# Optimization experiments

Hardware: AMD Instinct MI355X
Metric: run time of the kernel (lower is better)

The kernel has to match this reference:

```python
import jax, jax.numpy as jnp
import numpy as np

N_NODES = 100000
N_EDGES = 1200000
N_GRAPHS = 512
F_IN = 7
H = 64
N_CLASSES = 10


def _xavier(key, shape):
    fan_in, fan_out = shape[0], shape[1]
    limit = float(np.sqrt(6.0 / (fan_in + fan_out)))
    return jax.random.uniform(key, shape, jnp.float32, -limit, limit)


def setup_inputs() -> dict:
    key = jax.random.key(0)
    ks = jax.random.split(key, 16)
    x = jax.random.normal(ks[0], (N_NODES, F_IN), jnp.float32)
    edge_index = jax.random.randint(ks[1], (2, N_EDGES), 0, N_NODES, jnp.int64)
    batch = jnp.sort(jax.random.randint(ks[2], (N_NODES,), 0, N_GRAPHS, jnp.int64))
    d = {
        'x': x, 'edge_index': edge_index, 'batch': batch,
        'W_emb': _xavier(ks[3], (F_IN, H)), 'b_emb': jnp.zeros((H,), jnp.float32),
        'eps1': jnp.zeros((), jnp.float32),
        'W1a': _xavier(ks[4], (H, 2 * H)), 'b1a': jnp.zeros((2 * H,), jnp.float32),
        'W1b': _xavier(ks[5], (2 * H, H)), 'b1b': jnp.zeros((H,), jnp.float32),
        'eps2': jnp.zeros((), jnp.float32),
        'W2a': _xavier(ks[6], (H, 2 * H)), 'b2a': jnp.zeros((2 * H,), jnp.float32),
        'W2b': _xavier(ks[7], (2 * H, H)), 'b2b': jnp.zeros((H,), jnp.float32),
        'eps3': jnp.zeros((), jnp.float32),
        'W3a': _xavier(ks[8], (H, 2 * H)), 'b3a': jnp.zeros((2 * H,), jnp.float32),
        'W3b': _xavier(ks[9], (2 * H, H)), 'b3b': jnp.zeros((H,), jnp.float32),
        'Wc1': _xavier(ks[10], (2 * H, H)), 'bc1': jnp.zeros((H,), jnp.float32),
        'Wc2': _xavier(ks[11], (H, N_CLASSES)), 'bc2': jnp.zeros((N_CLASSES,), jnp.float32),
    }
    return d


def _gin_layer(x, eps, Wa, ba, Wb, bb, src, dst):
    # scatter-add aggregation of source features into destination nodes
    agg = jax.ops.segment_sum(x[src], dst, num_segments=N_NODES)
    h = (1.0 + eps) * x + agg
    h = jax.nn.relu(h @ Wa + ba) @ Wb + bb
    return jax.nn.elu(h)  # dropout is identity in eval mode


def reference(x, edge_index, batch,
              W_emb, b_emb,
              eps1, W1a, b1a, W1b, b1b,
              eps2, W2a, b2a, W2b, b2b,
              eps3, W3a, b3a, W3b, b3b,
              Wc1, bc1, Wc2, bc2):
    src, dst = edge_index[0], edge_index[1]
    h = x @ W_emb + b_emb                      # [N, H]
    h = _gin_layer(h, eps1, W1a, b1a, W1b, b1b, src, dst)
    h = _gin_layer(h, eps2, W2a, b2a, W2b, b2b, src, dst)
    h = _gin_layer(h, eps3, W3a, b3a, W3b, b3b, src, dst)
    # global mean + max pool per graph
    sums = jax.ops.segment_sum(h, batch, num_segments=N_GRAPHS)
    cnts = jax.ops.segment_sum(jnp.ones((h.shape[0], 1), h.dtype), batch, num_segments=N_GRAPHS)
    mean = sums / jnp.maximum(cnts, 1.0)
    mx = jax.ops.segment_max(h, batch, num_segments=N_GRAPHS)
    g = jnp.concatenate([mean, mx], axis=1)    # [G, 2H]
    out = jax.nn.relu(g @ Wc1 + bc1) @ Wc2 + bc2
    return out
```

## Files before the change

kernel.cpp:

```cpp
#include <hip/hip_runtime.h>
#include <hip/hip_bf16.h>
#include <math.h>

#define N_NODES 100000
#define N_EDGES 1200000
#define N_GRAPHS 512
#define NBUCKET 196
#define BSHIFT 9
#define TILE 2048
#define CSR_CAP 8192

typedef __bf16 bf16x8 __attribute__((ext_vector_type(8)));
typedef float f32x4 __attribute__((ext_vector_type(4)));

__device__ __forceinline__ unsigned f2ord(float f) {
  unsigned u = __float_as_uint(f);
  return (u & 0x80000000u) ? ~u : (u | 0x80000000u);
}
__device__ __forceinline__ float ord2f(unsigned u) {
  return (u & 0x80000000u) ? __uint_as_float(u & 0x7fffffffu) : __uint_as_float(~u);
}

__global__ void bucket_hist_kernel(const int* __restrict__ dst, int* __restrict__ bcnt) {
  __shared__ int c[256];
  int t = threadIdx.x;
  c[t] = 0;
  __syncthreads();
  for (int e = blockIdx.x * 256 + t; e < N_EDGES; e += gridDim.x * 256)
    atomicAdd(&c[dst[e] >> BSHIFT], 1);
  __syncthreads();
  if (t < NBUCKET && c[t] > 0) atomicAdd(&bcnt[t], c[t]);
}

__global__ void bucket_scan_kernel(const int* __restrict__ bcnt,
                                   int* __restrict__ bbase,
                                   int* __restrict__ bcursor,
                                   int* __restrict__ rowp) {
  __shared__ int s[256];
  int t = threadIdx.x;
  int own = (t < NBUCKET) ? bcnt[t] : 0;
  s[t] = own;
  __syncthreads();
  for (int o = 1; o < 256; o <<= 1) {
    int v = (t >= o) ? s[t - o] : 0;
    __syncthreads();
    s[t] += v;
    __syncthreads();
  }
  if (t < NBUCKET) {
    int excl = s[t] - own;
    bbase[t] = excl;
    bcursor[t] = excl;
  }
  if (t == 0) {
    bbase[NBUCKET] = N_EDGES;
    rowp[N_NODES] = N_EDGES;
  }
}

__global__ void partition_kernel(const int* __restrict__ src, const int* __restrict__ dst,
                                 int* __restrict__ bcursor, unsigned* __restrict__ ent) {
  __shared__ int cnt[256];
  __shared__ int cnt2[256];
  __shared__ int lstart[256];
  __shared__ int gbase[256];
  __shared__ int s[256];
  __shared__ unsigned sorted[TILE];
  __shared__ unsigned char bid[TILE];
  int t = threadIdx.x;
  int e0 = blockIdx.x * TILE;
  cnt[t] = 0; cnt2[t] = 0;
  __syncthreads();

  unsigned v[8];
  int b[8];
#pragma unroll
  for (int u = 0; u < 8; ++u) {
    int e = e0 + u * 256 + t;
    b[u] = -1;
    if (e < N_EDGES) {
      int d = dst[e];
      b[u] = d >> BSHIFT;
      v[u] = (unsigned)src[e] | ((unsigned)(d & 511) << 17);
      atomicAdd(&cnt[b[u]], 1);
    }
  }
  __syncthreads();
  s[t] = cnt[t];
  __syncthreads();
  for (int o = 1; o < 256; o <<= 1) {
    int x = (t >= o) ? s[t - o] : 0;
    __syncthreads();
    s[t] += x;
    __syncthreads();
  }
  lstart[t] = s[t] - cnt[t];
  __syncthreads();
  if (t < NBUCKET) gbase[t] = (cnt[t] > 0) ? atomicAdd(&bcursor[t], cnt[t]) : 0;
  __syncthreads();
#pragma unroll
  for (int u = 0; u < 8; ++u) {
    if (b[u] >= 0) {
      int p = lstart[b[u]] + atomicAdd(&cnt2[b[u]], 1);
      sorted[p] = v[u];
      bid[p] = (unsigned char)b[u];
    }
  }
  __syncthreads();
  int ntile = min(TILE, N_EDGES - e0);
  for (int i = t; i < ntile; i += 256) {
    int bb = bid[i];
    ent[gbase[bb] + (i - lstart[bb])] = sorted[i];
  }
}

__launch_bounds__(256)
__global__ void bucket_csr_kernel(const unsigned* __restrict__ ent,
                                  const int* __restrict__ bbase,
                                  int* __restrict__ rowp,
                                  int* __restrict__ ssrc) {
  __shared__ unsigned le[CSR_CAP];
  __shared__ int deg[512];
  __shared__ int excl[512];
  __shared__ int ws[256];
  int t = threadIdx.x;
  int b = blockIdx.x;
  int base = bbase[b];
  int cntb = bbase[b + 1] - base;
  deg[t] = 0; deg[t + 256] = 0;
  __syncthreads();
  for (int i = t; i < cntb; i += 256) {
    unsigned e = ent[base + i];
    if (i < CSR_CAP) le[i] = e;
    atomicAdd(&deg[e >> 17], 1);
  }
  __syncthreads();
  int d0 = deg[t * 2], d1 = deg[t * 2 + 1];
  int sum2 = d0 + d1;
  ws[t] = sum2;
  __syncthreads();
  for (int o = 1; o < 256; o <<= 1) {
    int x = (t >= o) ? ws[t - o] : 0;
    __syncthreads();
    ws[t] += x;
    __syncthreads();
  }
  int run = ws[t] - sum2;
  excl[t * 2] = run; run += d0;
  excl[t * 2 + 1] = run;
  __syncthreads();
  int node0 = b << BSHIFT;
#pragma unroll
  for (int k = 0; k < 2; ++k) {
    int i = t * 2 + k;
    int n = node0 + i;
    if (n < N_NODES) rowp[n] = base + excl[i];
    deg[i] = excl[i];
  }
  __syncthreads();
  for (int i = t; i < cntb; i += 256) {
    unsigned e = (i < CSR_CAP) ? le[i] : ent[base + i];
    int p = atomicAdd(&deg[e >> 17], 1);
    ssrc[base + p] = (int)(e & 0x1FFFFu);
  }
}

__global__ void convert_all_kernel(const float* __restrict__ W1a, const float* __restrict__ W1b,
                                   const float* __restrict__ W2a, const float* __restrict__ W2b,
                                   const float* __restrict__ W3a, const float* __restrict__ W3b,
                                   __bf16* __restrict__ wp,
                                   float* gsum, unsigned* gmax, int* gcnt) {
  int o = blockIdx.x * 256 + threadIdx.x;
  if (o < N_GRAPHS * 64) {
    gsum[o] = 0.0f;
    gmax[o] = 0x407FFFFFu;
  }
  if (o < N_GRAPHS) gcnt[o] = 0;
  int L = o >> 14, q = o & 16383;
  const float* Wa = (L == 0) ? W1a : (L == 1) ? W2a : W3a;
  const float* Wb = (L == 0) ? W1b : (L == 1) ? W2b : W3b;
  if (q < 8192) {
    int j = q & 7, c = (q >> 3) & 15, kc = (q >> 7) & 3, kt = (q >> 9) & 1, nt = q >> 10;
    wp[o] = (__bf16)Wa[(kt * 32 + kc * 8 + j) * 128 + nt * 16 + c];
  } else {
    int p = q - 8192;
    int j = p & 7, c = (p >> 3) & 15, kc = (p >> 7) & 3, kt = (p >> 9) & 3, nt2 = p >> 11;
    wp[o] = (__bf16)Wb[(kt * 32 + kc * 8 + j) * 64 + nt2 * 16 + c];
  }
}

__device__ __forceinline__ void mlp_tail(const __bf16* AsW, __bf16* HsW,
                                         const __bf16* __restrict__ W1p,
                                         const float* __restrict__ b1,
                                         const __bf16* __restrict__ W2p,
                                         const float* __restrict__ b2,
                                         __bf16* __restrict__ hout,
                                         int n0b, int wv, int c, int kc, int m0) {
  bf16x8 a1_0 = *(const bf16x8*)&AsW[(m0 + c) * 72 + 0 * 32 + kc * 8];
  bf16x8 a1_1 = *(const bf16x8*)&AsW[(m0 + c) * 72 + 1 * 32 + kc * 8];
  f32x4 acc1[8];
#pragma unroll
  for (int nt = 0; nt < 8; ++nt) {
    float bv = b1[nt * 16 + c];
    f32x4 acc = {bv, bv, bv, bv};
    bf16x8 bf0 = *(const bf16x8*)&W1p[(nt * 2 + 0) * 512 + kc * 128 + c * 8];
    bf16x8 bf1 = *(const bf16x8*)&W1p[(nt * 2 + 1) * 512 + kc * 128 + c * 8];
    acc = __builtin_amdgcn_mfma_f32_16x16x32_bf16(a1_0, bf0, acc, 0, 0, 0);
    acc = __builtin_amdgcn_mfma_f32_16x16x32_bf16(a1_1, bf1, acc, 0, 0, 0);
    acc1[nt] = acc;
  }
#pragma unroll
  for (int nt = 0; nt < 8; ++nt) {
#pragma unroll
    for (int r = 0; r < 4; ++r) {
      HsW[(m0 + kc * 4 + r) * 136 + nt * 16 + c] = (__bf16)fmaxf(acc1[nt][r], 0.0f);
    }
  }
  bf16x8 a2[4];
#pragma unroll
  for (int kt = 0; kt < 4; ++kt)
    a2[kt] = *(const bf16x8*)&HsW[(m0 + c) * 136 + kt * 32 + kc * 8];
#pragma unroll
  for (int nt2 = 0; nt2 < 4; ++nt2) {
    float bv = b2[nt2 * 16 + c];
    f32x4 acc = {bv, bv, bv, bv};
#pragma unroll
    for (int kt = 0; kt < 4; ++kt) {
      bf16x8 bf = *(const bf16x8*)&W2p[(nt2 * 4 + kt) * 512 + kc * 128 + c * 8];
      acc = __builtin_amdgcn_mfma_f32_16x16x32_bf16(a2[kt], bf, acc, 0, 0, 0);
    }
#pragma unroll
    for (int r = 0; r < 4; ++r) {
      int g = n0b + m0 + kc * 4 + r;
      if (g < N_NODES) {
        float o = acc[r];
        hout[(size_t)g * 64 + nt2 * 16 + c] = (__bf16)((o > 0.0f) ? o : expm1f(o));
      }
    }
  }
}

__launch_bounds__(256)
__global__ void gin_fused_l1_kernel(const float* __restrict__ x,
                                    __bf16* __restrict__ hout,
                                    const int* __restrict__ row_ptr,
                                    const int* __restrict__ ssrc,
                                    const float* __restrict__ eps_p,
                                    const float* __restrict__ W_emb,
                                    const float* __restrict__ b_emb,
                                    const __bf16* __restrict__ W1p,
                                    const float* __restrict__ b1,
                                    const __bf16* __restrict__ W2p,
                                    const float* __restrict__ b2) {
  __shared__ __bf16 As[64 * 72];
  __shared__ __bf16 Hs[64 * 136];
  int t = threadIdx.x, lane = t & 63, wv = t >> 6;
  int c = lane & 15, kc = lane >> 4;
  int m0 = wv * 16;
  float epsv = 1.0f + eps_p[0];
  int n0b = blockIdx.x * 64;
  int n0w = n0b + m0;

  float w0 = W_emb[0 * 64 + lane], w1 = W_emb[1 * 64 + lane], w2 = W_emb[2 * 64 + lane];
  float w3 = W_emb[3 * 64 + lane], w4 = W_emb[4 * 64 + lane], w5 = W_emb[5 * 64 + lane];
  float w6 = W_emb[6 * 64 + lane];
  float bl = b_emb[lane];

  int rp = row_ptr[min(n0w + min(lane, 16), N_NODES)];

#define EDGE7(sv, acc) { \
    const float* xr = &x[(size_t)(sv) * 7]; \
    acc = fmaf(xr[0], w0, acc); acc = fmaf(xr[1], w1, acc); \
    acc = fmaf(xr[2], w2, acc); acc = fmaf(xr[3], w3, acc); \
    acc = fmaf(xr[4], w4, acc); acc = fmaf(xr[5], w5, acc); \
    acc = fmaf(xr[6], w6, acc); }

  for (int r = 0; r < 16; ++r) {
    int n = n0w + r;
    float acc = 0.0f;
    if (n < N_NODES) {
      int j = __builtin_amdgcn_readfirstlane(__shfl(rp, r));
      int e = __builtin_amdgcn_readfirstlane(__shfl(rp, r + 1));
      acc = bl * (epsv + (float)(e - j));
      const float* xn = &x[(size_t)n * 7];
      float s0x = epsv * xn[0], s1x = epsv * xn[1], s2x = epsv * xn[2];
      float s3x = epsv * xn[3], s4x = epsv * xn[4], s5x = epsv * xn[5];
      float s6x = epsv * xn[6];
      acc = fmaf(s0x, w0, acc); acc = fmaf(s1x, w1, acc); acc = fmaf(s2x, w2, acc);
      acc = fmaf(s3x, w3, acc); acc = fmaf(s4x, w4, acc); acc = fmaf(s5x, w5, acc);
      acc = fmaf(s6x, w6, acc);
      for (; j + 2 <= e; j += 2) {
        int sa = ssrc[j], sb = ssrc[j + 1];
        EDGE7(sa, acc);
        EDGE7(sb, acc);
      }
      if (j < e) { int sa = ssrc[j]; EDGE7(sa, acc); }
    }
    As[(m0 + r) * 72 + lane] = (__bf16)acc;
  }
#undef EDGE7

  mlp_tail(As, Hs, W1p, b1, W2p, b2, hout, n0b, wv, c, kc, m0);
}

__launch_bounds__(256)
__global__ void gin_fused5_kernel(const __bf16* __restrict__ hin,
                                  __bf16* __restrict__ hout,
                                  const int* __restrict__ row_ptr,
                                  const int* __restrict__ ssrc,
                                  const float* __restrict__ eps_p,
                                  const __bf16* __restrict__ W1p,
                                  const float* __restrict__ b1,
                                  const __bf16* __restrict__ W2p,
                                  const float* __restrict__ b2) {
  __shared__ __bf16 As[64 * 72];
  __shared__ __bf16 Hs[64 * 136];
  int t = threadIdx.x, lane = t & 63, wv = t >> 6;
  int c = lane & 15, kc = lane >> 4;
  int m0 = wv * 16;
  float epsv = 1.0f + eps_p[0];
  int n0b = blockIdx.x * 64;
  int n0w = n0b + m0;

  int rp = row_ptr[min(n0w + min(lane, 16), N_NODES)];

#define DRAIN(j, e, acc) \
  while (j + 4 <= e) { \
    int q0 = ssrc[j], q1 = ssrc[j + 1], q2 = ssrc[j + 2], q3 = ssrc[j + 3]; \
    float g0 = (float)hin[(size_t)q0 * 64 + lane]; \
    float g1 = (float)hin[(size_t)q1 * 64 + lane]; \
    float g2 = (float)hin[(size_t)q2 * 64 + lane]; \
    float g3 = (float)hin[(size_t)q3 * 64 + lane]; \
    acc += (g0 + g1) + (g2 + g3); j += 4; \
  } \
  for (; j < e; ++j) acc += (float)hin[(size_t)ssrc[j] * 64 + lane];

  for (int rq = 0; rq < 4; ++rq) {
    int r0 = rq, r1 = rq + 4, r2 = rq + 8, r3 = rq + 12;
    int n0 = n0w + r0, n1 = n0w + r1, n2 = n0w + r2, n3 = n0w + r3;
    int j0 = __builtin_amdgcn_readfirstlane(__shfl(rp, r0));
    int e0 = __builtin_amdgcn_readfirstlane(__shfl(rp, r0 + 1));
    int j1 = __builtin_amdgcn_readfirstlane(__shfl(rp, r1));
    int e1 = __builtin_amdgcn_readfirstlane(__shfl(rp, r1 + 1));
    int j2 = __builtin_amdgcn_readfirstlane(__shfl(rp, r2));
    int e2 = __builtin_amdgcn_readfirstlane(__shfl(rp, r2 + 1));
    int j3 = __builtin_amdgcn_readfirstlane(__shfl(rp, r3));
    int e3 = __builtin_amdgcn_readfirstlane(__shfl(rp, r3 + 1));
    float a0 = (n0 < N_NODES) ? epsv * (float)hin[(size_t)n0 * 64 + lane] : 0.0f;
    float a1 = (n1 < N_NODES) ? epsv * (float)hin[(size_t)n1 * 64 + lane] : 0.0f;
    float a2 = (n2 < N_NODES) ? epsv * (float)hin[(size_t)n2 * 64 + lane] : 0.0f;
    float a3 = (n3 < N_NODES) ? epsv * (float)hin[(size_t)n3 * 64 + lane] : 0.0f;
    while (j0 + 4 <= e0 && j1 + 4 <= e1 && j2 + 4 <= e2 && j3 + 4 <= e3) {
      int s00 = ssrc[j0], s01 = ssrc[j0 + 1], s02 = ssrc[j0 + 2], s03 = ssrc[j0 + 3];
      int s10 = ssrc[j1], s11 = ssrc[j1 + 1], s12 = ssrc[j1 + 2], s13 = ssrc[j1 + 3];
      int s20 = ssrc[j2], s21 = ssrc[j2 + 1], s22 = ssrc[j2 + 2], s23 = ssrc[j2 + 3];
      int s30 = ssrc[j3], s31 = ssrc[j3 + 1], s32 = ssrc[j3 + 2], s33 = ssrc[j3 + 3];
      float f00 = (float)hin[(size_t)s00 * 64 + lane];
      float f01 = (float)hin[(size_t)s01 * 64 + lane];
      float f02 = (float)hin[(size_t)s02 * 64 + lane];
      float f03 = (float)hin[(size_t)s03 * 64 + lane];
      float f10 = (float)hin[(size_t)s10 * 64 + lane];
      float f11 = (float)hin[(size_t)s11 * 64 + lane];
      float f12 = (float)hin[(size_t)s12 * 64 + lane];
      float f13 = (float)hin[(size_t)s13 * 64 + lane];
      float f20 = (float)hin[(size_t)s20 * 64 + lane];
      float f21 = (float)hin[(size_t)s21 * 64 + lane];
      float f22 = (float)hin[(size_t)s22 * 64 + lane];
      float f23 = (float)hin[(size_t)s23 * 64 + lane];
      float f30 = (float)hin[(size_t)s30 * 64 + lane];
      float f31 = (float)hin[(size_t)s31 * 64 + lane];
      float f32_ = (float)hin[(size_t)s32 * 64 + lane];
      float f33 = (float)hin[(size_t)s33 * 64 + lane];
      a0 += (f00 + f01) + (f02 + f03);
      a1 += (f10 + f11) + (f12 + f13);
      a2 += (f20 + f21) + (f22 + f23);
      a3 += (f30 + f31) + (f32_ + f33);
      j0 += 4; j1 += 4; j2 += 4; j3 += 4;
    }
    DRAIN(j0, e0, a0);
    DRAIN(j1, e1, a1);
    DRAIN(j2, e2, a2);
    DRAIN(j3, e3, a3);
    As[(m0 + r0) * 72 + lane] = (__bf16)a0;
    As[(m0 + r1) * 72 + lane] = (__bf16)a1;
    As[(m0 + r2) * 72 + lane] = (__bf16)a2;
    As[(m0 + r3) * 72 + lane] = (__bf16)a3;
  }
#undef DRAIN

  mlp_tail(As, Hs, W1p, b1, W2p, b2, hout, n0b, wv, c, kc, m0);
}

__global__ void pool_kernel(const __bf16* __restrict__ h,
                            const int* __restrict__ batch,
                            float* gsum, unsigned* gmax, int* gcnt) {
  int lane = threadIdx.x & 63;
  int wave = (blockIdx.x * blockDim.x + threadIdx.x) >> 6;
  int nwaves = (gridDim.x * blockDim.x) >> 6;
  int chunk = (N_NODES + nwaves - 1) / nwaves;
  int n0 = wave * chunk;
  int n1 = min(n0 + chunk, N_NODES);
  if (n0 >= N_NODES) return;
  int cur = batch[n0];
  float s = 0.0f, m = -2.0f;
  int cnt = 0;
  for (int n = n0; n < n1; ++n) {
    int g = batch[n];
    if (g != cur) {
      atomicAdd(&gsum[cur * 64 + lane], s);
      atomicMax(&gmax[cur * 64 + lane], f2ord(m));
      if (lane == 0) atomicAdd(&gcnt[cur], cnt);
      cur = g; s = 0.0f; m = -2.0f; cnt = 0;
    }
    float v = (float)h[(size_t)n * 64 + lane];
    s += v;
    m = fmaxf(m, v);
    ++cnt;
  }
  atomicAdd(&gsum[cur * 64 + lane], s);
  atomicMax(&gmax[cur * 64 + lane], f2ord(m));
  if (lane == 0) atomicAdd(&gcnt[cur], cnt);
}

__global__ void cls_kernel(const float* __restrict__ gsum,
                           const unsigned* __restrict__ gmax,
                           const int* __restrict__ gcnt,
                           const float* __restrict__ Wc1,
                           const float* __restrict__ bc1,
                           const float* __restrict__ Wc2,
                           const float* __restrict__ bc2,
                           float* __restrict__ out) {
  __shared__ float gv[128];
  __shared__ float tv[64];
  int g = blockIdx.x, l = threadIdx.x;
  float cnt = fmaxf((float)gcnt[g], 1.0f);
  gv[l] = gsum[g * 64 + l] / cnt;
  gv[64 + l] = ord2f(gmax[g * 64 + l]);
  __syncthreads();
  float acc = bc1[l];
#pragma unroll 8
  for (int k = 0; k < 128; ++k) acc = fmaf(gv[k], Wc1[k * 64 + l], acc);
  tv[l] = fmaxf(acc, 0.0f);
  __syncthreads();
  if (l < 10) {
    float o = bc2[l];
#pragma unroll
    for (int k = 0; k < 64; ++k) o = fmaf(tv[k], Wc2[k * 10 + l], o);
    out[g * 10 + l] = o;
  }
}

extern "C" void kernel_launch(void* const* d_in, const int* in_sizes, int n_in,
                              void* d_out, int out_size, void* d_ws, size_t ws_size,
                              hipStream_t stream) {
  const float* x     = (const float*)d_in[0];
  const int*   ei    = (const int*)d_in[1];
  const int*   batch = (const int*)d_in[2];
  const float* W_emb = (const float*)d_in[3];
  const float* b_emb = (const float*)d_in[4];
  const float* eps1  = (const float*)d_in[5];
  const float* W1a   = (const float*)d_in[6];
  const float* b1a   = (const float*)d_in[7];
  const float* W1b   = (const float*)d_in[8];
  const float* b1b   = (const float*)d_in[9];
  const float* eps2  = (const float*)d_in[10];
  const float* W2a   = (const float*)d_in[11];
  const float* b2a   = (const float*)d_in[12];
  const float* W2b   = (const float*)d_in[13];
  const float* b2b   = (const float*)d_in[14];
  const float* eps3  = (const float*)d_in[15];
  const float* W3a   = (const float*)d_in[16];
  const float* b3a   = (const float*)d_in[17];
  const float* W3b   = (const float*)d_in[18];
  const float* b3b   = (const float*)d_in[19];
  const float* Wc1   = (const float*)d_in[20];
  const float* bc1   = (const float*)d_in[21];
  const float* Wc2   = (const float*)d_in[22];
  const float* bc2   = (const float*)d_in[23];
  float* out = (float*)d_out;

  char* w = (char*)d_ws;
  __bf16*   h0   = (__bf16*)w;                     w += (size_t)N_NODES * 64 * 2;
  __bf16*   h1   = (__bf16*)w;                     w += (size_t)N_NODES * 64 * 2;
  float*    gsum = (float*)w;                      w += N_GRAPHS * 64 * 4;
  unsigned* gmax = (unsigned*)w;                   w += N_GRAPHS * 64 * 4;
  int*      gcnt = (int*)w;                        w += N_GRAPHS * 4;
  __bf16*   wp   = (__bf16*)w;                     w += 3 * 16384 * 2;
  int*      bcnt = (int*)w;                        w += 256 * 4;
  int*      bbase= (int*)w;                        w += 260 * 4;
  int*      bcur = (int*)w;                        w += 256 * 4;
  int*      rowp = (int*)w;                        w += (size_t)(N_NODES + 1) * 4;
  unsigned* ent  = (unsigned*)w;                   w += (size_t)N_EDGES * 4;
  int*      ssrc = (int*)w;                        w += (size_t)N_EDGES * 4;

  const int* src = ei;
  const int* dst = ei + N_EDGES;

  hipMemsetAsync(bcnt, 0, 256 * sizeof(int), stream);
  bucket_hist_kernel<<<256, 256, 0, stream>>>(dst, bcnt);
  bucket_scan_kernel<<<1, 256, 0, stream>>>(bcnt, bbase, bcur, rowp);
  partition_kernel<<<(N_EDGES + TILE - 1) / TILE, 256, 0, stream>>>(src, dst, bcur, ent);
  bucket_csr_kernel<<<NBUCKET, 256, 0, stream>>>(ent, bbase, rowp, ssrc);

  convert_all_kernel<<<192, 256, 0, stream>>>(W1a, W1b, W2a, W2b, W3a, W3b, wp,
                                              gsum, gmax, gcnt);

  const int NGB = (N_NODES + 63) / 64;
  gin_fused_l1_kernel<<<NGB, 256, 0, stream>>>(
      x, h0, rowp, ssrc, eps1, W_emb, b_emb,
      wp + 0 * 16384, b1a, wp + 0 * 16384 + 8192, b1b);
  gin_fused5_kernel<<<NGB, 256, 0, stream>>>(
      h0, h1, rowp, ssrc, eps2,
      wp + 1 * 16384, b2a, wp + 1 * 16384 + 8192, b2b);
  gin_fused5_kernel<<<NGB, 256, 0, stream>>>(
      h1, h0, rowp, ssrc, eps3,
      wp + 2 * 16384, b3a, wp + 2 * 16384 + 8192, b3b);

  pool_kernel<<<512, 256, 0, stream>>>(h0, batch, gsum, gmax, gcnt);
  cls_kernel<<<N_GRAPHS, 64, 0, stream>>>(gsum, gmax, gcnt, Wc1, bc1, Wc2, bc2, out);
}
```

Before: 446.6 us.

## Precompute node embeddings separately and unroll pool loop by four

```diff
diff --git a/kernel.cpp b/kernel.cpp
--- a/kernel.cpp
+++ b/kernel.cpp
@@ -165,6 +165,25 @@
   }
 }
 
+__global__ void embed_kernel(const float* __restrict__ x,
+                             const float* __restrict__ W,
+                             const float* __restrict__ b,
+                             __bf16* __restrict__ h) {
+  __shared__ float Ws[7 * 64];
+  __shared__ float bs[64];
+  int t = threadIdx.x;
+  for (int i = t; i < 7 * 64; i += 256) Ws[i] = W[i];
+  if (t < 64) bs[t] = b[t];
+  __syncthreads();
+  int gid = blockIdx.x * 256 + t;
+  int n = gid >> 6, f = gid & 63;
+  const float* xr = x + n * 7;
+  float acc = bs[f];
+#pragma unroll
+  for (int k = 0; k < 7; ++k) acc = fmaf(xr[k], Ws[k * 64 + f], acc);
+  h[gid] = (__bf16)acc;
+}
+
 __global__ void convert_all_kernel(const float* __restrict__ W1a, const float* __restrict__ W1b,
                                    const float* __restrict__ W2a, const float* __restrict__ W2b,
                                    const float* __restrict__ W3a, const float* __restrict__ W3b,
@@ -238,69 +257,6 @@
       }
     }
   }
-}
-
-__launch_bounds__(256)
-__global__ void gin_fused_l1_kernel(const float* __restrict__ x,
-                                    __bf16* __restrict__ hout,
-                                    const int* __restrict__ row_ptr,
-                                    const int* __restrict__ ssrc,
-                                    const float* __restrict__ eps_p,
-                                    const float* __restrict__ W_emb,
-                                    const float* __restrict__ b_emb,
-                                    const __bf16* __restrict__ W1p,
-                                    const float* __restrict__ b1,
-                                    const __bf16* __restrict__ W2p,
-                                    const float* __restrict__ b2) {
-  __shared__ __bf16 As[64 * 72];
-  __shared__ __bf16 Hs[64 * 136];
-  int t = threadIdx.x, lane = t & 63, wv = t >> 6;
-  int c = lane & 15, kc = lane >> 4;
-  int m0 = wv * 16;
-  float epsv = 1.0f + eps_p[0];
-  int n0b = blockIdx.x * 64;
-  int n0w = n0b + m0;
-
-  float w0 = W_emb[0 * 64 + lane], w1 = W_emb[1 * 64 + lane], w2 = W_emb[2 * 64 + lane];
-  float w3 = W_emb[3 * 64 + lane], w4 = W_emb[4 * 64 + lane], w5 = W_emb[5 * 64 + lane];
-  float w6 = W_emb[6 * 64 + lane];
-  float bl = b_emb[lane];
-
-  int rp = row_ptr[min(n0w + min(lane, 16), N_NODES)];
-
-#define EDGE7(sv, acc) { \
-    const float* xr = &x[(size_t)(sv) * 7]; \
-    acc = fmaf(xr[0], w0, acc); acc = fmaf(xr[1], w1, acc); \
-    acc = fmaf(xr[2], w2, acc); acc = fmaf(xr[3], w3, acc); \
-    acc = fmaf(xr[4], w4, acc); acc = fmaf(xr[5], w5, acc); \
-    acc = fmaf(xr[6], w6, acc); }
-
-  for (int r = 0; r < 16; ++r) {
-    int n = n0w + r;
-    float acc = 0.0f;
-    if (n < N_NODES) {
-      int j = __builtin_amdgcn_readfirstlane(__shfl(rp, r));
-      int e = __builtin_amdgcn_readfirstlane(__shfl(rp, r + 1));
-      acc = bl * (epsv + (float)(e - j));
-      const float* xn = &x[(size_t)n * 7];
-      float s0x = epsv * xn[0], s1x = epsv * xn[1], s2x = epsv * xn[2];
-      float s3x = epsv * xn[3], s4x = epsv * xn[4], s5x = epsv * xn[5];
-      float s6x = epsv * xn[6];
-      acc = fmaf(s0x, w0, acc); acc = fmaf(s1x, w1, acc); acc = fmaf(s2x, w2, acc);
-      acc = fmaf(s3x, w3, acc); acc = fmaf(s4x, w4, acc); acc = fmaf(s5x, w5, acc);
-      acc = fmaf(s6x, w6, acc);
-      for (; j + 2 <= e; j += 2) {
-        int sa = ssrc[j], sb = ssrc[j + 1];
-        EDGE7(sa, acc);
-        EDGE7(sb, acc);
-      }
-      if (j < e) { int sa = ssrc[j]; EDGE7(sa, acc); }
-    }
-    As[(m0 + r) * 72 + lane] = (__bf16)acc;
-  }
-#undef EDGE7
-
-  mlp_tail(As, Hs, W1p, b1, W2p, b2, hout, n0b, wv, c, kc, m0);
 }
 
 __launch_bounds__(256)
@@ -404,19 +360,32 @@
   int cur = batch[n0];
   float s = 0.0f, m = -2.0f;
   int cnt = 0;
-  for (int n = n0; n < n1; ++n) {
+#define POOL_ONE(g, v)                                         \
+  if (g != cur) {                                              \
+    atomicAdd(&gsum[cur * 64 + lane], s);                      \
+    atomicMax(&gmax[cur * 64 + lane], f2ord(m));               \
+    if (lane == 0) atomicAdd(&gcnt[cur], cnt);                 \
+    cur = g; s = 0.0f; m = -2.0f; cnt = 0;                     \
+  }                                                            \
+  s += v; m = fmaxf(m, v); ++cnt;
+  int n = n0;
+  for (; n + 4 <= n1; n += 4) {
+    int g0 = batch[n], g1 = batch[n + 1], g2 = batch[n + 2], g3 = batch[n + 3];
+    float v0 = (float)h[(size_t)n * 64 + lane];
+    float v1 = (float)h[(size_t)(n + 1) * 64 + lane];
+    float v2 = (float)h[(size_t)(n + 2) * 64 + lane];
+    float v3 = (float)h[(size_t)(n + 3) * 64 + lane];
+    POOL_ONE(g0, v0);
+    POOL_ONE(g1, v1);
+    POOL_ONE(g2, v2);
+    POOL_ONE(g3, v3);
+  }
+  for (; n < n1; ++n) {
     int g = batch[n];
-    if (g != cur) {
-      atomicAdd(&gsum[cur * 64 + lane], s);
-      atomicMax(&gmax[cur * 64 + lane], f2ord(m));
-      if (lane == 0) atomicAdd(&gcnt[cur], cnt);
-      cur = g; s = 0.0f; m = -2.0f; cnt = 0;
-    }
     float v = (float)h[(size_t)n * 64 + lane];
-    s += v;
-    m = fmaxf(m, v);
-    ++cnt;
-  }
+    POOL_ONE(g, v);
+  }
+#undef POOL_ONE
   atomicAdd(&gsum[cur * 64 + lane], s);
   atomicMax(&gmax[cur * 64 + lane], f2ord(m));
   if (lane == 0) atomicAdd(&gcnt[cur], cnt);
@@ -496,6 +465,10 @@
   const int* src = ei;
   const int* dst = ei + N_EDGES;
 
+  const float* epss[3] = {eps1, eps2, eps3};
+  const float* bas[3]  = {b1a, b2a, b3a};
+  const float* bbs[3]  = {b1b, b2b, b3b};
+
   hipMemsetAsync(bcnt, 0, 256 * sizeof(int), stream);
   bucket_hist_kernel<<<256, 256, 0, stream>>>(dst, bcnt);
   bucket_scan_kernel<<<1, 256, 0, stream>>>(bcnt, bbase, bcur, rowp);
@@ -504,18 +477,17 @@
 
   convert_all_kernel<<<192, 256, 0, stream>>>(W1a, W1b, W2a, W2b, W3a, W3b, wp,
                                               gsum, gmax, gcnt);
+  embed_kernel<<<(N_NODES * 64) / 256, 256, 0, stream>>>(x, W_emb, b_emb, h0);
 
   const int NGB = (N_NODES + 63) / 64;
-  gin_fused_l1_kernel<<<NGB, 256, 0, stream>>>(
-      x, h0, rowp, ssrc, eps1, W_emb, b_emb,
-      wp + 0 * 16384, b1a, wp + 0 * 16384 + 8192, b1b);
-  gin_fused5_kernel<<<NGB, 256, 0, stream>>>(
-      h0, h1, rowp, ssrc, eps2,
-      wp + 1 * 16384, b2a, wp + 1 * 16384 + 8192, b2b);
-  gin_fused5_kernel<<<NGB, 256, 0, stream>>>(
-      h1, h0, rowp, ssrc, eps3,
-      wp + 2 * 16384, b3a, wp + 2 * 16384 + 8192, b3b);
-
-  pool_kernel<<<512, 256, 0, stream>>>(h0, batch, gsum, gmax, gcnt);
+  __bf16* hbuf[4] = {h0, h1, h0, h1};
+  for (int L = 0; L < 3; ++L) {
+    gin_fused5_kernel<<<NGB, 256, 0, stream>>>(
+        hbuf[L], hbuf[L + 1], rowp, ssrc, epss[L],
+        wp + (size_t)L * 16384, bas[L],
+        wp + (size_t)L * 16384 + 8192, bbs[L]);
+  }
+
+  pool_kernel<<<512, 256, 0, stream>>>(h1, batch, gsum, gmax, gcnt);
   cls_kernel<<<N_GRAPHS, 64, 0, stream>>>(gsum, gmax, gcnt, Wc1, bc1, Wc2, bc2, out);
 }
```

Result: faster. 398.5 us (-10.8%).
